# Kernel tuning notes

Hardware: AMD Instinct MI355X
Metric: run time of the kernel (lower is better)

Reference implementation:

```python
import jax, jax.numpy as jnp
import numpy as np

B, NR, NL, M = 1, 512, 256, 4
IN_C, MID, OUT_C = 256, 32, 128


def layer_norm(x, g, b):
    mu = jnp.mean(x, axis=-1, keepdims=True)
    xc = x - mu
    var = jnp.mean(xc * xc, axis=-1, keepdims=True)
    return xc * jax.lax.rsqrt(var + 1e-5) * g + b


def setup_inputs() -> dict:
    key = jax.random.key(0)
    ks = jax.random.split(key, 12)
    s = 0.02
    f32 = jnp.float32
    return {
        "rec_1d": jax.random.normal(ks[0], (B, NR, IN_C), f32),
        "lig_1d": jax.random.normal(ks[1], (B, M, NL, IN_C), f32),
        "pw_rep": jax.random.normal(ks[2], (B, NR + NL, NR + NL, OUT_C), f32),
        "r_norm_g": jnp.ones((IN_C,), f32), "r_norm_b": jnp.zeros((IN_C,), f32),
        "l_norm_g": jnp.ones((IN_C,), f32), "l_norm_b": jnp.zeros((IN_C,), f32),
        "W_r": jax.random.normal(ks[3], (MID * 4, IN_C), f32) * s, "b_r": jnp.zeros((MID * 4,), f32),
        "W_l": jax.random.normal(ks[4], (MID * 4, IN_C), f32) * s, "b_l": jnp.zeros((MID * 4,), f32),
        "W_rr": jax.random.normal(ks[5], (OUT_C, MID * MID), f32) * s, "b_rr": jnp.zeros((OUT_C,), f32),
        "W_rl": jax.random.normal(ks[6], (OUT_C, MID * MID), f32) * s, "b_rl": jnp.zeros((OUT_C,), f32),
        "W_lr": jax.random.normal(ks[7], (OUT_C, MID * MID), f32) * s, "b_lr": jnp.zeros((OUT_C,), f32),
        "W_ll": jax.random.normal(ks[8], (OUT_C, MID * MID), f32) * s, "b_ll": jnp.zeros((OUT_C,), f32),
    }


def reference(rec_1d, lig_1d, pw_rep, r_norm_g, r_norm_b, l_norm_g, l_norm_b,
              W_r, b_r, W_l, b_l, W_rr, b_rr, W_rl, b_rl, W_lr, b_lr, W_ll, b_ll):
    m = lig_1d.shape[1]          # number of ligand symmetry copies
    nr = rec_1d.shape[1]         # number of receptor residues
    mid = W_r.shape[0] // 4
    out_c = W_rr.shape[0]

    rec = layer_norm(rec_1d, r_norm_g, r_norm_b)
    lig = layer_norm(lig_1d, l_norm_g, l_norm_b)

    # projections -> [..., mid, 4]; torch.chunk + [..., -1] picks slices 0..3
    pr = (rec @ W_r.T + b_r).reshape(rec.shape[0], rec.shape[1], mid, 4)
    pl = (lig @ W_l.T + b_l).reshape(lig.shape[0], m, lig.shape[2], mid, 4)
    r_ri, r_rj, r_li, r_lj = pr[..., 0], pr[..., 1], pr[..., 2], pr[..., 3]
    l_ri, l_rj, l_li, l_lj = pl[..., 0], pl[..., 1], pl[..., 2], pl[..., 3]

    Wrr = W_rr.reshape(out_c, mid, mid)
    Wrl = W_rl.reshape(out_c, mid, mid)
    Wlr = W_lr.reshape(out_c, mid, mid)
    Wll = W_ll.reshape(out_c, mid, mid)

    # r_li/r_lj are broadcast over m in the original; the /m sum is a mean over copies
    l_ri_m = jnp.mean(l_ri, axis=1)  # [B, Nl, mid]
    l_rj_m = jnp.mean(l_rj, axis=1)

    # Algebraically identical to final_linear(outer(a,c).flatten(-2)):
    # contract the final weight with the j-side first, avoiding O(N^2*mid^2) tensors.
    t = jnp.einsum('bjy,oxy->bjox', r_rj, Wrr)
    rr = jnp.einsum('bix,bjox->bijo', r_ri, t) + b_rr            # [B, Nr, Nr, out]
    t = jnp.einsum('bjy,oxy->bjox', l_rj_m, Wrl)
    rl = jnp.einsum('bix,bjox->bijo', r_li, t) + b_rl            # [B, Nr, Nl, out]
    t = jnp.einsum('bjy,oxy->bjox', l_ri_m, Wlr)
    lr = jnp.einsum('bix,bjox->bjio', r_lj, t) + b_lr            # [B, Nl, Nr, out]
    t = jnp.einsum('bmjy,oxy->bmjox', l_lj, Wll)
    ll = jnp.einsum('bmix,bmjox->bijo', l_li, t) / m + b_ll      # [B, Nl, Nl, out]

    pw = jnp.zeros_like(pw_rep)
    pw = pw.at[:, :nr, :nr].set(rr)
    pw = pw.at[:, :nr, nr:].set(rl)
    pw = pw.at[:, nr:, :nr].set(lr)
    pw = pw.at[:, nr:, nr:].set(ll)
    return pw
```

## Files before the change

kernel.cpp:

```cpp
#include <hip/hip_runtime.h>

constexpr int IN_C  = 256;
constexpr int MID   = 32;
constexpr int OUT_C = 128;
constexpr int NR    = 512;
constexpr int NL    = 256;
constexpr int M     = 4;
constexpr long ROW_STRIDE = (long)(NR + NL) * OUT_C;

constexpr long WS_PR4 = 0;
constexpr long WS_PL4 = WS_PR4 + 4L * NR * MID;
constexpr long WS_F32_END = WS_PL4 + 4L * M * NL * MID;
constexpr long BF_LRR = 2 * WS_F32_END;
constexpr long BF_LRL = BF_LRR + (long)NR * MID;
constexpr long BF_LLR = BF_LRL + (long)NR * MID;
constexpr long BF_LLL = BF_LLR + (long)NR * MID;
constexpr long BF_TRR = BF_LLL + (long)NL * M * MID;
constexpr long BF_TRL = BF_TRR + (long)NR * OUT_C * MID;
constexpr long BF_TLR = BF_TRL + (long)NL * OUT_C * MID;
constexpr long BF_TLL = BF_TLR + (long)NL * OUT_C * MID;

typedef __bf16 bf16x8 __attribute__((ext_vector_type(8)));
typedef float  f32x4  __attribute__((ext_vector_type(4)));

__device__ inline unsigned short f2bf(float f) {
    unsigned int u = __float_as_uint(f);
    u = (u + 0x7fffu + ((u >> 16) & 1u)) >> 16;
    return (unsigned short)u;
}

union BF8 { unsigned int u[4]; bf16x8 v; };

__global__ __launch_bounds__(256) void ln_proj_kernel(
    const float* __restrict__ rec, const float* __restrict__ lig,
    const float* __restrict__ rg, const float* __restrict__ rb,
    const float* __restrict__ lg, const float* __restrict__ lb,
    const float* __restrict__ Wr, const float* __restrict__ br,
    const float* __restrict__ Wl, const float* __restrict__ bl,
    float* __restrict__ ws)
{
    __shared__ unsigned int xn4[16 * 128];
    int bid = blockIdx.x;
    int rowbase = bid * 16;
    bool isRec = (rowbase < NR);
    const float* X    = isRec ? rec + (long)rowbase * IN_C
                              : lig + (long)(rowbase - NR) * IN_C;
    const float* g    = isRec ? rg : lg;
    const float* bv   = isRec ? rb : lb;
    const float* W    = isRec ? Wr : Wl;
    const float* bias = isRec ? br : bl;

    int tid = threadIdx.x;
    {
        int rl = tid >> 4, p = tid & 15;
        const float* xp = X + (long)rl * IN_C + p * 16;
        float4 xv[4];
        float s = 0.f, s2 = 0.f;
        #pragma unroll
        for (int q = 0; q < 4; ++q) {
            xv[q] = *(const float4*)(xp + q * 4);
            s  += xv[q].x + xv[q].y + xv[q].z + xv[q].w;
            s2 += xv[q].x*xv[q].x + xv[q].y*xv[q].y + xv[q].z*xv[q].z + xv[q].w*xv[q].w;
        }
        #pragma unroll
        for (int m = 1; m < 16; m <<= 1) {
            s  += __shfl_xor(s,  m, 64);
            s2 += __shfl_xor(s2, m, 64);
        }
        float mu = s * (1.f / IN_C);
        float var = s2 * (1.f / IN_C) - mu * mu;
        float rs = rsqrtf(var + 1e-5f);
        #pragma unroll
        for (int q = 0; q < 4; ++q) {
            int k0 = p * 16 + q * 4;
            float4 gv = *(const float4*)(g + k0);
            float4 bb = *(const float4*)(bv + k0);
            float n0 = (xv[q].x - mu) * rs * gv.x + bb.x;
            float n1 = (xv[q].y - mu) * rs * gv.y + bb.y;
            float n2 = (xv[q].z - mu) * rs * gv.z + bb.z;
            float n3 = (xv[q].w - mu) * rs * gv.w + bb.w;
            int idx  = rl * 128 + (k0 >> 1);
            int sidx = idx ^ ((rl & 7) << 2);
            xn4[sidx]     = (unsigned)f2bf(n0) | ((unsigned)f2bf(n1) << 16);
            xn4[sidx + 1] = (unsigned)f2bf(n2) | ((unsigned)f2bf(n3) << 16);
        }
    }
    __syncthreads();

    int wv = tid >> 6, l = tid & 63;
    int lrow = l & 15, lk = l >> 4;
    int ob = wv * 32;

    f32x4 acc0 = *(const f32x4*)(bias + ob + lk * 4);
    f32x4 acc1 = *(const f32x4*)(bias + ob + 16 + lk * 4);

    for (int ks = 0; ks < 8; ++ks) {
        int idx = (lrow * 128 + ks * 16 + lk * 4) ^ ((lrow & 7) << 2);
        bf16x8 xf = *(const bf16x8*)&xn4[idx];
        const float* w0 = W + (long)(ob + lrow) * IN_C + ks * 32 + lk * 8;
        const float* w1 = w0 + 16L * IN_C;
        float4 a0 = *(const float4*)w0, a1 = *(const float4*)(w0 + 4);
        float4 c0 = *(const float4*)w1, c1 = *(const float4*)(w1 + 4);
        BF8 wf0, wf1;
        wf0.u[0] = (unsigned)f2bf(a0.x) | ((unsigned)f2bf(a0.y) << 16);
        wf0.u[1] = (unsigned)f2bf(a0.z) | ((unsigned)f2bf(a0.w) << 16);
        wf0.u[2] = (unsigned)f2bf(a1.x) | ((unsigned)f2bf(a1.y) << 16);
        wf0.u[3] = (unsigned)f2bf(a1.z) | ((unsigned)f2bf(a1.w) << 16);
        wf1.u[0] = (unsigned)f2bf(c0.x) | ((unsigned)f2bf(c0.y) << 16);
        wf1.u[1] = (unsigned)f2bf(c0.z) | ((unsigned)f2bf(c0.w) << 16);
        wf1.u[2] = (unsigned)f2bf(c1.x) | ((unsigned)f2bf(c1.y) << 16);
        wf1.u[3] = (unsigned)f2bf(c1.z) | ((unsigned)f2bf(c1.w) << 16);
        acc0 = __builtin_amdgcn_mfma_f32_16x16x32_bf16(wf0.v, xf, acc0, 0, 0, 0);
        acc1 = __builtin_amdgcn_mfma_f32_16x16x32_bf16(wf1.v, xf, acc1, 0, 0, 0);
    }

    unsigned short* wsb = (unsigned short*)ws;
    int prow = isRec ? (rowbase + lrow) : (rowbase - NR + lrow);
    long slice_stride = isRec ? (long)NR * MID : (long)M * NL * MID;
    float* P4 = isRec ? (ws + WS_PR4) : (ws + WS_PL4);
    #pragma unroll
    for (int t = 0; t < 2; ++t) {
        f32x4 acc = t ? acc1 : acc0;
        int xi = (ob >> 2) + t * 4 + lk;
        #pragma unroll
        for (int r = 0; r < 4; ++r) {
            float val = acc[r];
            P4[(long)r * slice_stride + (long)prow * MID + xi] = val;
            unsigned short hb = f2bf(val);
            if (isRec) {
                if (r == 0)      wsb[BF_LRR + (long)prow * 32 + xi] = hb;
                else if (r == 2) wsb[BF_LRL + (long)prow * 32 + xi] = hb;
                else if (r == 3) wsb[BF_LLR + (long)prow * 32 + xi] = hb;
            } else if (r == 2) {
                wsb[BF_LLL + (long)(prow & 255) * 128 + (prow >> 8) * 32 + xi] = hb;
            }
        }
    }
}

__global__ __launch_bounds__(256) void build_t_kernel(
    const float* __restrict__ Wrr, const float* __restrict__ Wrl,
    const float* __restrict__ Wlr, const float* __restrict__ Wll,
    float* __restrict__ ws)
{
    __shared__ unsigned int Vs[512 * 16];
    __shared__ unsigned int Wsh[64 * 16];
    unsigned short* wsb = (unsigned short*)ws;
    const float* V4 = ws + WS_PL4;
    int bid = blockIdx.x;
    int tid = threadIdx.x;

    int mode, cblk, jhalf = 0, Vrows;
    const float* W;
    unsigned short* T;
    if (bid < 64)       { mode = 0; cblk = bid;       W = Wrr; T = wsb + BF_TRR; Vrows = 512; }
    else if (bid < 128) { mode = 1; cblk = bid - 64;  W = Wrl; T = wsb + BF_TRL; Vrows = 256; }
    else if (bid < 192) { mode = 2; cblk = bid - 128; W = Wlr; T = wsb + BF_TLR; Vrows = 256; }
    else                { mode = 3; int r = bid - 192; cblk = r >> 1; jhalf = r & 1;
                          W = Wll; T = wsb + BF_TLL; Vrows = 512; }

    for (int f = tid; f < Vrows * 4; f += 256) {
        int row = f >> 2, blk = f & 3;
        int y0 = blk * 8;
        float vals[8];
        if (mode == 0) {
            const float* p = ws + WS_PR4 + (long)NR * MID + (long)row * 32 + y0;
            #pragma unroll
            for (int i = 0; i < 8; ++i) vals[i] = p[i];
        } else if (mode == 3) {
            const float* p = V4 + 3L * M * NL * MID + (long)(jhalf * 512 + row) * 32 + y0;
            #pragma unroll
            for (int i = 0; i < 8; ++i) vals[i] = 0.25f * p[i];
        } else {
            int sl = (mode == 1) ? 1 : 0;
            const float* p = V4 + (long)sl * M * NL * MID + (long)row * 32 + y0;
            #pragma unroll
            for (int i = 0; i < 8; ++i)
                vals[i] = 0.25f * (p[i] + p[8192 + i] + p[16384 + i] + p[24576 + i]);
        }
        unsigned int* dst = &Vs[row * 16 + ((blk ^ (row & 3)) << 2)];
        #pragma unroll
        for (int q = 0; q < 4; ++q)
            dst[q] = (unsigned)f2bf(vals[2*q]) | ((unsigned)f2bf(vals[2*q+1]) << 16);
    }
    {
        int row = tid >> 2, blk = tid & 3;
        const float* p = W + (long)(cblk * 64 + row) * 32 + blk * 8;
        float4 a = *(const float4*)p, b = *(const float4*)(p + 4);
        unsigned int* dst = &Wsh[row * 16 + ((blk ^ (row & 3)) << 2)];
        dst[0] = (unsigned)f2bf(a.x) | ((unsigned)f2bf(a.y) << 16);
        dst[1] = (unsigned)f2bf(a.z) | ((unsigned)f2bf(a.w) << 16);
        dst[2] = (unsigned)f2bf(b.x) | ((unsigned)f2bf(b.y) << 16);
        dst[3] = (unsigned)f2bf(b.z) | ((unsigned)f2bf(b.w) << 16);
    }
    __syncthreads();

    int wv = tid >> 6, l = tid & 63;
    int lrow = l & 15, lk = l >> 4;
    int wrow = wv * 16 + lrow;
    bf16x8 af = *(const bf16x8*)&Wsh[wrow * 16 + ((lk ^ (wrow & 3)) << 2)];
    int c0 = cblk * 64 + wv * 16 + lk * 4;

    int nj = Vrows >> 4;
    for (int jt = 0; jt < nj; ++jt) {
        int vr = jt * 16 + lrow;
        bf16x8 bf = *(const bf16x8*)&Vs[vr * 16 + ((lk ^ (vr & 3)) << 2)];
        f32x4 acc = {0.f, 0.f, 0.f, 0.f};
        acc = __builtin_amdgcn_mfma_f32_16x16x32_bf16(af, bf, acc, 0, 0, 0);
        unsigned long long pk =
              (unsigned long long)f2bf(acc[0])
            | ((unsigned long long)f2bf(acc[1]) << 16)
            | ((unsigned long long)f2bf(acc[2]) << 32)
            | ((unsigned long long)f2bf(acc[3]) << 48);
        if (mode < 3) {
            *(unsigned long long*)(T + (long)vr * 4096 + c0) = pk;
        } else {
            int vg = jhalf * 512 + vr;
            int m = vg >> 8, j = vg & 255;
            *(unsigned long long*)(T + (long)j * 16384 + ((c0 >> 5) << 7) + m * 32 + (c0 & 31)) = pk;
        }
    }
}

template<int K>
__device__ inline void epi_wave(const unsigned short* __restrict__ L,
                                const unsigned short* __restrict__ T,
                                const float* __restrict__ bias,
                                float* __restrict__ obrow,
                                long istr, int i0, int lrow, int lk)
{
    constexpr int NK = K / 32;
    bf16x8 bl0[NK], bl1[NK];
    #pragma unroll
    for (int ks = 0; ks < NK; ++ks) {
        int kb = ks * 32 + lk * 8;
        bl0[ks] = *(const bf16x8*)(L + (long)(i0 + lrow) * K + kb);
        bl1[ks] = *(const bf16x8*)(L + (long)(i0 + 16 + lrow) * K + kb);
    }
    f32x4 acc[2][8];
    #pragma unroll
    for (int of = 0; of < 8; ++of) {
        f32x4 b4 = *(const f32x4*)(bias + of * 16 + lk * 4);
        acc[0][of] = b4; acc[1][of] = b4;
    }
    #pragma unroll
    for (int ks = 0; ks < NK; ++ks) {
        int kb = ks * 32 + lk * 8;
        #pragma unroll
        for (int of = 0; of < 8; ++of) {
            bf16x8 a = *(const bf16x8*)(T + (long)(of * 16 + lrow) * K + kb);
            acc[0][of] = __builtin_amdgcn_mfma_f32_16x16x32_bf16(a, bl0[ks], acc[0][of], 0, 0, 0);
            acc[1][of] = __builtin_amdgcn_mfma_f32_16x16x32_bf16(a, bl1[ks], acc[1][of], 0, 0, 0);
        }
    }
    float* obase = obrow + (long)lk * 4;
    #pragma unroll
    for (int fi = 0; fi < 2; ++fi) {
        long ibase = (long)(i0 + fi * 16 + lrow) * istr;
        #pragma unroll
        for (int of = 0; of < 8; ++of) {
            *(f32x4*)(obase + ibase + of * 16) = acc[fi][of];
        }
    }
}

__global__ __launch_bounds__(256) void epilogue_kernel(
    const float* __restrict__ ws, float* __restrict__ out,
    const float* __restrict__ brr, const float* __restrict__ brl,
    const float* __restrict__ blr, const float* __restrict__ bll)
{
    const unsigned short* wsb = (const unsigned short*)ws;
    int bid = blockIdx.x;
    int x = bid & 7;
    int r = bid >> 3;

    const unsigned short *L, *Tq;
    const float* bias;
    float* ob;
    long istr, jstr;
    int j0, i0b, quadK;
    if (r < 128) {
        int jw = r & 15, it = r >> 4;
        j0 = x * 64 + jw * 4; i0b = it * 64; quadK = 32;
        L = wsb + BF_LRR; Tq = wsb + BF_TRR; bias = brr;
        ob = out; jstr = 128; istr = ROW_STRIDE;
    } else if (r < 192) {
        int w = r - 128; int jw = w & 7, it = w >> 3;
        j0 = x * 32 + jw * 4; i0b = it * 64; quadK = 32;
        L = wsb + BF_LRL; Tq = wsb + BF_TRL; bias = brl;
        ob = out + (long)NR * OUT_C; jstr = 128; istr = ROW_STRIDE;
    } else if (r < 256) {
        int w = r - 192; int jw = w & 7, it = w >> 3;
        j0 = x * 32 + jw * 4; i0b = it * 64; quadK = 32;
        L = wsb + BF_LLR; Tq = wsb + BF_TLR; bias = blr;
        ob = out + (long)NR * ROW_STRIDE; jstr = ROW_STRIDE; istr = 128;
    } else {
        int w = r - 256; int jw = w & 7, it = w >> 3;
        j0 = x * 32 + jw * 4; i0b = it * 64; quadK = 128;
        L = wsb + BF_LLL; Tq = wsb + BF_TLL; bias = bll;
        ob = out + (long)NR * ROW_STRIDE + (long)NR * OUT_C; jstr = 128; istr = ROW_STRIDE;
    }

    int tid = threadIdx.x;
    int wv = tid >> 6, l = tid & 63;
    int lrow = l & 15, lk = l >> 4;
    int j = j0 + wv;

    if (quadK == 32) {
        const unsigned short* T = Tq + (long)j * 4096;
        float* obj = ob + (long)j * jstr;
        #pragma unroll
        for (int ic = 0; ic < 2; ++ic)
            epi_wave<32>(L, T, bias, obj, istr, i0b + ic * 32, lrow, lk);
    } else {
        const unsigned short* T = Tq + (long)j * 16384;
        float* obj = ob + (long)j * jstr;
        #pragma unroll
        for (int ic = 0; ic < 2; ++ic)
            epi_wave<128>(L, T, bias, obj, istr, i0b + ic * 32, lrow, lk);
    }
}

extern "C" void kernel_launch(void* const* d_in, const int* in_sizes, int n_in,
                              void* d_out, int out_size, void* d_ws, size_t ws_size,
                              hipStream_t stream)
{
    (void)in_sizes; (void)n_in; (void)out_size; (void)ws_size;
    const float* rec = (const float*)d_in[0];
    const float* lig = (const float*)d_in[1];
    const float* rg  = (const float*)d_in[3];
    const float* rb  = (const float*)d_in[4];
    const float* lg  = (const float*)d_in[5];
    const float* lb  = (const float*)d_in[6];
    const float* Wr  = (const float*)d_in[7];
    const float* br  = (const float*)d_in[8];
    const float* Wl  = (const float*)d_in[9];
    const float* bl  = (const float*)d_in[10];
    const float* Wrr = (const float*)d_in[11];
    const float* brr = (const float*)d_in[12];
    const float* Wrl = (const float*)d_in[13];
    const float* brl = (const float*)d_in[14];
    const float* Wlr = (const float*)d_in[15];
    const float* blr = (const float*)d_in[16];
    const float* Wll = (const float*)d_in[17];
    const float* bll = (const float*)d_in[18];
    float* out = (float*)d_out;
    float* ws  = (float*)d_ws;

    hipLaunchKernelGGL(ln_proj_kernel, dim3(96), dim3(256), 0, stream,
                       rec, lig, rg, rb, lg, lb, Wr, br, Wl, bl, ws);
    hipLaunchKernelGGL(build_t_kernel, dim3(320), dim3(256), 0, stream,
                       Wrr, Wrl, Wlr, Wll, ws);
    hipLaunchKernelGGL(epilogue_kernel, dim3(2304), dim3(256), 0, stream,
                       ws, out, brr, brl, blr, bll);
}
```

Measured before the change: 90.71 us.

## Restructure epilogue into per-row sweeps over j with swapped MFMA operands

Adds an epi_sweep path in which each wave keeps a 16-row slice of L and the bias in registers. The wave then iterates over a block of j columns, issuing MFMAs with T as the A operand so each lane writes contiguous output rows. The rr, rl and ll quadrants use this sweep, while lr keeps the old epi_wave path with two j per wave. The grid drops from 2304 to 1024 blocks. The aim is to reuse L loads across many j and to get more coalesced output stores, at the cost of fewer blocks and a longer serial loop per wave.

```diff
diff --git a/kernel.cpp b/kernel.cpp
--- a/kernel.cpp
+++ b/kernel.cpp
@@ -222,6 +222,41 @@
     }
 }
 
+template<int K, int JB>
+__device__ inline void epi_sweep(
+    const unsigned short* __restrict__ L,
+    const unsigned short* __restrict__ T0,
+    const float* __restrict__ bias,
+    float* __restrict__ ob,
+    int i0, int lrow, int lk, int wv)
+{
+    constexpr int NK = K / 32;
+    bf16x8 bl[NK];
+    #pragma unroll
+    for (int ks = 0; ks < NK; ++ks)
+        bl[ks] = *(const bf16x8*)(L + (long)(i0 + lrow) * K + ks * 32 + lk * 8);
+    f32x4 b4[8];
+    #pragma unroll
+    for (int of = 0; of < 8; ++of)
+        b4[of] = *(const f32x4*)(bias + of * 16 + lk * 4);
+    float* orow = ob + (long)(i0 + lrow) * ROW_STRIDE + lk * 4;
+    for (int s = 0; s < JB / 4; ++s) {
+        int j = s * 4 + wv;
+        const unsigned short* T = T0 + (long)j * (K * 128);
+        float* oj = orow + (long)j * 128;
+        #pragma unroll
+        for (int of = 0; of < 8; ++of) {
+            f32x4 acc = b4[of];
+            #pragma unroll
+            for (int ks = 0; ks < NK; ++ks) {
+                bf16x8 a = *(const bf16x8*)(T + (long)(of * 16 + lrow) * K + ks * 32 + lk * 8);
+                acc = __builtin_amdgcn_mfma_f32_16x16x32_bf16(a, bl[ks], acc, 0, 0, 0);
+            }
+            *(f32x4*)(oj + of * 16) = acc;
+        }
+    }
+}
+
 template<int K>
 __device__ inline void epi_wave(const unsigned short* __restrict__ L,
                                 const unsigned short* __restrict__ T,
@@ -274,50 +309,38 @@
     int x = bid & 7;
     int r = bid >> 3;
 
-    const unsigned short *L, *Tq;
-    const float* bias;
-    float* ob;
-    long istr, jstr;
-    int j0, i0b, quadK;
-    if (r < 128) {
-        int jw = r & 15, it = r >> 4;
-        j0 = x * 64 + jw * 4; i0b = it * 64; quadK = 32;
-        L = wsb + BF_LRR; Tq = wsb + BF_TRR; bias = brr;
-        ob = out; jstr = 128; istr = ROW_STRIDE;
-    } else if (r < 192) {
-        int w = r - 128; int jw = w & 7, it = w >> 3;
-        j0 = x * 32 + jw * 4; i0b = it * 64; quadK = 32;
-        L = wsb + BF_LRL; Tq = wsb + BF_TRL; bias = brl;
-        ob = out + (long)NR * OUT_C; jstr = 128; istr = ROW_STRIDE;
-    } else if (r < 256) {
-        int w = r - 192; int jw = w & 7, it = w >> 3;
-        j0 = x * 32 + jw * 4; i0b = it * 64; quadK = 32;
-        L = wsb + BF_LLR; Tq = wsb + BF_TLR; bias = blr;
-        ob = out + (long)NR * ROW_STRIDE; jstr = ROW_STRIDE; istr = 128;
-    } else {
-        int w = r - 256; int jw = w & 7, it = w >> 3;
-        j0 = x * 32 + jw * 4; i0b = it * 64; quadK = 128;
-        L = wsb + BF_LLL; Tq = wsb + BF_TLL; bias = bll;
-        ob = out + (long)NR * ROW_STRIDE + (long)NR * OUT_C; jstr = 128; istr = ROW_STRIDE;
-    }
-
     int tid = threadIdx.x;
     int wv = tid >> 6, l = tid & 63;
     int lrow = l & 15, lk = l >> 4;
-    int j = j0 + wv;
-
-    if (quadK == 32) {
-        const unsigned short* T = Tq + (long)j * 4096;
-        float* obj = ob + (long)j * jstr;
-        #pragma unroll
-        for (int ic = 0; ic < 2; ++ic)
-            epi_wave<32>(L, T, bias, obj, istr, i0b + ic * 32, lrow, lk);
+
+    if (r < 32) {
+        int i0 = r * 16, j0 = x * 64;
+        epi_sweep<32, 64>(wsb + BF_LRR, wsb + BF_TRR + (long)j0 * 4096, brr,
+                          out + (long)j0 * 128, i0, lrow, lk, wv);
+    } else if (r < 64) {
+        int i0 = (r - 32) * 16, j0 = x * 32;
+        epi_sweep<32, 32>(wsb + BF_LRL, wsb + BF_TRL + (long)j0 * 4096, brl,
+                          out + (long)NR * OUT_C + (long)j0 * 128, i0, lrow, lk, wv);
+    } else if (r < 96) {
+        int w = r - 64; int it = w & 7, jw = w >> 3;
+        int j0 = x * 32 + jw * 8, i0b = it * 64;
+        const unsigned short* L = wsb + BF_LLR;
+        float* ob = out + (long)NR * ROW_STRIDE;
+        #pragma unroll
+        for (int jj = 0; jj < 2; ++jj) {
+            int j = j0 + jj * 4 + wv;
+            const unsigned short* T = wsb + BF_TLR + (long)j * 4096;
+            float* obj = ob + (long)j * ROW_STRIDE;
+            #pragma unroll
+            for (int ic = 0; ic < 2; ++ic)
+                epi_wave<32>(L, T, blr, obj, 128, i0b + ic * 32, lrow, lk);
+        }
     } else {
-        const unsigned short* T = Tq + (long)j * 16384;
-        float* obj = ob + (long)j * jstr;
-        #pragma unroll
-        for (int ic = 0; ic < 2; ++ic)
-            epi_wave<128>(L, T, bias, obj, istr, i0b + ic * 32, lrow, lk);
+        int w = r - 96; int it = w & 15, jw = w >> 4;
+        int i0 = it * 16, j0 = x * 32 + jw * 16;
+        epi_sweep<128, 16>(wsb + BF_LLL, wsb + BF_TLL + (long)j0 * 16384, bll,
+                           out + (long)NR * ROW_STRIDE + (long)NR * OUT_C + (long)j0 * 128,
+                           i0, lrow, lk, wv);
     }
 }
 
@@ -351,6 +374,6 @@
                        rec, lig, rg, rb, lg, lb, Wr, br, Wl, bl, ws);
     hipLaunchKernelGGL(build_t_kernel, dim3(320), dim3(256), 0, stream,
                        Wrr, Wrl, Wlr, Wll, ws);
-    hipLaunchKernelGGL(epilogue_kernel, dim3(2304), dim3(256), 0, stream,
+    hipLaunchKernelGGL(epilogue_kernel, dim3(1024), dim3(256), 0, stream,
                        ws, out, brr, brl, blr, bll);
 }
```

New measurement: 110.7 us. +22.0%, slower.
